# Performance work log

Measured on AMD Instinct MI355X. Metric: run time of the kernel, lower is better.

## Reference

```python
import jax, jax.numpy as jnp
import numpy as np

N_R = 256          # number of relations
N_HOP_MAX = 3      # max hops
N_E = 200_000      # number of entities
N_T = 1_000_000    # number of KB triples
B = 32             # batch size
D_Q = 768          # BERT question embedding dim
D_IN = D_Q + (N_HOP_MAX - 1) * N_R  # input width of dense_inf / dense_att


def setup_inputs() -> dict:
    key = jax.random.key(0)
    ks = jax.random.split(key, 7)
    x = (jax.random.uniform(ks[0], (B, N_E)) < 0.001).astype(jnp.float32)
    h_q = jax.random.normal(ks[1], (B, D_Q), jnp.float32)
    W_inf = jax.random.normal(ks[2], (N_R, D_IN), jnp.float32) * 0.02
    W_att = jax.random.normal(ks[3], (1, D_IN), jnp.float32) * 0.02
    subj_idx = jax.random.randint(ks[4], (N_T,), 0, N_E, jnp.int32)
    rel_idx = jax.random.randint(ks[5], (N_T,), 0, N_R, jnp.int32)
    obj_idx = jax.random.randint(ks[6], (N_T,), 0, N_E, jnp.int32)
    return {"x": x, "h_q": h_q, "W_inf": W_inf, "W_att": W_att,
            "subj_idx": subj_idx, "rel_idx": rel_idx, "obj_idx": obj_idx,
            "n_hop": N_HOP_MAX}


def _one_step(x, r, subj_idx, rel_idx, obj_idx):
    # Equivalent to ((x @ M_subj.T) * (r @ M_rel.T)) @ M_obj with 0/1
    # indicator matrices: gather - elementwise multiply - scatter-add.
    x_t = jnp.take(x, subj_idx, axis=1)   # (B, N_T)
    r_t = jnp.take(r, rel_idx, axis=1)    # (B, N_T)
    prod = x_t * r_t                       # (B, N_T)
    # scatter-add over triples into object entities: (N_T, B) -> (N_E, B)
    return jax.ops.segment_sum(prod.T, obj_idx, num_segments=x.shape[1]).T


def reference(x, h_q, W_inf, W_att, subj_idx, rel_idx, obj_idx, n_hop):
    rs, cs, xs = [], [], []
    for i in range(n_hop):
        if i:
            # most-recent relation first, then older ones (rs[::-1])
            concat = jnp.concatenate([h_q] + rs[::-1], axis=1)
        else:
            concat = h_q
        pad = jnp.zeros((h_q.shape[0], (N_HOP_MAX - 1 - i) * N_R), h_q.dtype)
        concat = jnp.concatenate([concat, pad], axis=1)  # (B, D_IN)
        r = concat @ W_inf.T   # (B, N_R)
        c = concat @ W_att.T   # (B, 1)
        x = _one_step(x, r, subj_idx, rel_idx, obj_idx)  # (B, N_E)
        rs.append(r)
        cs.append(c)
        xs.append(x)
    a = jax.nn.softmax(jnp.concatenate(cs, axis=1), axis=-1)  # (B, n_hop)
    y = jnp.einsum('bh,bhe->be', a, jnp.stack(xs, axis=1))     # (B, N_E)
    return y
```

## Files before the change

kernel.cpp:

```cpp
#include <hip/hip_runtime.h>

#define N_R   256
#define N_E   200000
#define N_T   1000000
#define D_Q   768
#define D_IN  1280

template <bool BN>
__device__ __forceinline__ void hop_quad(
        const float* __restrict__ xIn, const unsigned* __restrict__ maskIn,
        const float* __restrict__ rT,
        const int4* __restrict__ subj4, const int4* __restrict__ rel4,
        const int4* __restrict__ obj4,
        float* __restrict__ xOut, unsigned* __restrict__ maskOut,
        int gb, int t) {
    int tid = gb * 256 + t;
    if (tid >= N_T / 4) return;
    int4 s4 = subj4[tid];
    unsigned m0 = maskIn[s4.x], m1 = maskIn[s4.y];
    unsigned m2 = maskIn[s4.z], m3 = maskIn[s4.w];
    if (!(m0 | m1 | m2 | m3)) return;
    int4 r4 = rel4[tid];
    int4 o4 = obj4[tid];
    int      ss[4] = {s4.x, s4.y, s4.z, s4.w};
    unsigned mk[4] = {m0, m1, m2, m3};
    int      rr[4] = {r4.x, r4.y, r4.z, r4.w};
    int      oo[4] = {o4.x, o4.y, o4.z, o4.w};
#pragma unroll
    for (int k = 0; k < 4; ++k) {
        unsigned mm = mk[k];
        if (!mm) continue;
        int s = ss[k], o = oo[k];
        const float* rrow = rT + rr[k] * 32;
        while (mm) {
            int bb = __ffs(mm) - 1;
            mm &= mm - 1;
            float v = BN ? xIn[(size_t)bb * N_E + s] : xIn[(size_t)s * 32 + bb];
            unsafeAtomicAdd(&xOut[(size_t)o * 32 + bb], v * rrow[bb]);
        }
        atomicOr(&maskOut[o], mk[k]);
    }
}

__global__ void kA(const float* __restrict__ x, const float* __restrict__ h_q,
                   const float* __restrict__ W_inf,
                   unsigned* __restrict__ mask0, unsigned* __restrict__ mask1,
                   unsigned* __restrict__ mask2,
                   float4* __restrict__ outv, float* __restrict__ rT0) {
    __shared__ float hs[32 * 257];
    __shared__ float red[256];
    int t = threadIdx.x;
    if (blockIdx.x < 782) {
        int tid = blockIdx.x * 256 + t;
        float4 z = {0.f, 0.f, 0.f, 0.f};
        for (int i = tid; i < 1600000; i += 782 * 256) outv[i] = z;
        if (tid < N_E) {
            unsigned m = 0;
#pragma unroll 8
            for (int b = 0; b < 32; ++b)
                m |= (x[(size_t)b * N_E + tid] != 0.f ? 1u : 0u) << b;
            mask0[tid] = m;
            mask1[tid] = 0u;
            mask2[tid] = 0u;
        }
    } else {
        int rel = blockIdx.x - 782;
        int b = t & 31, kp = t >> 5;
        float acc = 0.f;
        for (int c = 0; c < 3; ++c) {
            __syncthreads();
#pragma unroll
            for (int i = 0; i < 32; ++i)
                hs[i * 257 + t] = h_q[i * D_Q + c * 256 + t];
            __syncthreads();
            const float* w = &W_inf[rel * D_IN + c * 256 + kp * 32];
#pragma unroll
            for (int i = 0; i < 32; ++i)
                acc += w[i] * hs[b * 257 + kp * 32 + i];
        }
        red[t] = acc;
        __syncthreads();
        if (t < 32) {
            float s = 0.f;
            for (int q = 0; q < 8; ++q) s += red[q * 32 + t];
            rT0[rel * 32 + t] = s;
        }
    }
}

__global__ void kB(const float* __restrict__ W_inf, const float* __restrict__ rT0,
                   float* __restrict__ rT1,
                   const float* __restrict__ x, const unsigned* __restrict__ mask0,
                   const int4* __restrict__ subj4, const int4* __restrict__ rel4,
                   const int4* __restrict__ obj4,
                   float* __restrict__ bufA, unsigned* __restrict__ mask1) {
    __shared__ float red[256];
    int t = threadIdx.x;
    if (blockIdx.x < 256) {
        int relb = blockIdx.x;
        int b = t & 31, jp = t >> 5;
        const float* w2 = &W_inf[relb * D_IN + D_Q];
        float acc = 0.f;
#pragma unroll 8
        for (int jj = 0; jj < 32; ++jj) {
            int j = jp * 32 + jj;
            acc += w2[j] * rT0[j * 32 + b];
        }
        red[t] = acc;
        __syncthreads();
        if (t < 32) {
            float s = rT0[relb * 32 + t];
            for (int q = 0; q < 8; ++q) s += red[q * 32 + t];
            rT1[relb * 32 + t] = s;
        }
    } else {
        hop_quad<true>(x, mask0, rT0, subj4, rel4, obj4, bufA, mask1,
                       blockIdx.x - 256, t);
    }
}

__global__ void kC(const float* __restrict__ W_inf, const float* __restrict__ W_att,
                   const float* __restrict__ h_q,
                   const float* __restrict__ rT0, const float* __restrict__ rT1,
                   float* __restrict__ rT2, float* __restrict__ a_w,
                   const float* __restrict__ bufA, const unsigned* __restrict__ mask1,
                   const int4* __restrict__ subj4, const int4* __restrict__ rel4,
                   const int4* __restrict__ obj4,
                   float* __restrict__ bufB, unsigned* __restrict__ mask2,
                   float* __restrict__ out) {
    __shared__ float red[256];
    __shared__ float p0[256], p1[256], p2[256], p3[256];
    int t = threadIdx.x;
    if (blockIdx.x < 256) {
        int relb = blockIdx.x;
        int b = t & 31, jp = t >> 5;
        const float* w2 = &W_inf[relb * D_IN + D_Q];
        const float* w3 = w2 + N_R;
        float acc = 0.f;
#pragma unroll 8
        for (int jj = 0; jj < 32; ++jj) {
            int j = jp * 32 + jj;
            acc += w2[j] * rT1[j * 32 + b] + w3[j] * rT0[j * 32 + b];
        }
        red[t] = acc;
        __syncthreads();
        if (t < 32) {
            float s = rT0[relb * 32 + t];
            for (int q = 0; q < 8; ++q) s += red[q * 32 + t];
            rT2[relb * 32 + t] = s;
        }
    } else if (blockIdx.x == 256) {
        int b = t & 31, p = t >> 5;
        float c0 = 0.f;
        for (int k = p * 96; k < p * 96 + 96; ++k) c0 += W_att[k] * h_q[b * D_Q + k];
        float s1 = 0.f, s2 = 0.f, s3 = 0.f;
        for (int j = p * 32; j < p * 32 + 32; ++j) {
            float w2 = W_att[D_Q + j], w3 = W_att[D_Q + N_R + j];
            float r0v = rT0[j * 32 + b], r1v = rT1[j * 32 + b];
            s1 += w2 * r0v; s2 += w2 * r1v; s3 += w3 * r0v;
        }
        p0[t] = c0; p1[t] = s1; p2[t] = s2; p3[t] = s3;
        __syncthreads();
        if (t < 32) {
            float C0 = 0.f, S1 = 0.f, S2 = 0.f, S3 = 0.f;
            for (int q = 0; q < 8; ++q) {
                C0 += p0[q * 32 + t]; S1 += p1[q * 32 + t];
                S2 += p2[q * 32 + t]; S3 += p3[q * 32 + t];
            }
            float c1 = C0 + S1, c2 = C0 + S2 + S3;
            float m  = fmaxf(C0, fmaxf(c1, c2));
            float e0 = __expf(C0 - m), e1 = __expf(c1 - m), e2 = __expf(c2 - m);
            float inv = 1.f / (e0 + e1 + e2);
            a_w[t] = e0 * inv; a_w[32 + t] = e1 * inv; a_w[64 + t] = e2 * inv;
        }
    } else if (blockIdx.x < 1234) {
        hop_quad<false>(bufA, mask1, rT1, subj4, rel4, obj4, bufB, mask2,
                        blockIdx.x - 257, t);
    } else {
        __shared__ float a0l[32];
        if (t < 32) {
            int b = t;
            float c0 = 0.f;
            for (int k = 0; k < D_Q; ++k) c0 += W_att[k] * h_q[b * D_Q + k];
            float s1 = 0.f, s2 = 0.f, s3 = 0.f;
            for (int j = 0; j < N_R; ++j) {
                float w2 = W_att[D_Q + j], w3 = W_att[D_Q + N_R + j];
                float r0v = rT0[j * 32 + b], r1v = rT1[j * 32 + b];
                s1 += w2 * r0v; s2 += w2 * r1v; s3 += w3 * r0v;
            }
            float C0 = c0, c1 = C0 + s1, c2 = C0 + s2 + s3;
            float m  = fmaxf(C0, fmaxf(c1, c2));
            float e0 = __expf(C0 - m), e1 = __expf(c1 - m), e2 = __expf(c2 - m);
            a0l[t] = e0 / (e0 + e1 + e2);
        }
        __syncthreads();
        int e = (blockIdx.x - 1234) * 256 + t;
        if (e >= N_E) return;
        unsigned m1v = mask1[e];
        if (!m1v) return;
        const float* r1 = bufA + (size_t)e * 32;
        while (m1v) {
            int bb = __ffs(m1v) - 1;
            m1v &= m1v - 1;
            unsafeAtomicAdd(&out[(size_t)bb * N_E + e], a0l[bb] * r1[bb]);
        }
    }
}

__global__ void kDE(const float* __restrict__ bufB,
                    const unsigned* __restrict__ mask2,
                    const float* __restrict__ rT2, const float* __restrict__ a_w,
                    const int2* __restrict__ subj2, const int2* __restrict__ rel2,
                    const int2* __restrict__ obj2, float* __restrict__ out) {
    __shared__ float a1s[32], a2s[32];
    int t = threadIdx.x;
    if (t < 32) { a1s[t] = a_w[32 + t]; a2s[t] = a_w[64 + t]; }
    __syncthreads();
    if (blockIdx.x < 1954) {
        int tid = blockIdx.x * 256 + t;
        if (tid >= N_T / 2) return;
        int2 s2 = subj2[tid];
        unsigned m0 = mask2[s2.x], m1 = mask2[s2.y];
        if (!(m0 | m1)) return;
        int2 r2 = rel2[tid];
        int2 o2 = obj2[tid];
        int      ss[2] = {s2.x, s2.y};
        unsigned mk[2] = {m0, m1};
        int      rr[2] = {r2.x, r2.y};
        int      oo[2] = {o2.x, o2.y};
#pragma unroll
        for (int k = 0; k < 2; ++k) {
            unsigned mm = mk[k];
            if (!mm) continue;
            const float* rrow = rT2 + rr[k] * 32;
            const float* xrow = bufB + (size_t)ss[k] * 32;
            int o = oo[k];
            while (mm) {
                int bb = __ffs(mm) - 1;
                mm &= mm - 1;
                unsafeAtomicAdd(&out[(size_t)bb * N_E + o],
                                a2s[bb] * xrow[bb] * rrow[bb]);
            }
        }
    } else {
        int e = (blockIdx.x - 1954) * 256 + t;
        if (e >= N_E) return;
        unsigned m2v = mask2[e];
        if (!m2v) return;
        const float* r2 = bufB + (size_t)e * 32;
        while (m2v) {
            int bb = __ffs(m2v) - 1;
            m2v &= m2v - 1;
            unsafeAtomicAdd(&out[(size_t)bb * N_E + e], a1s[bb] * r2[bb]);
        }
    }
}

extern "C" void kernel_launch(void* const* d_in, const int* in_sizes, int n_in,
                              void* d_out, int out_size, void* d_ws, size_t ws_size,
                              hipStream_t stream) {
    const float* x     = (const float*)d_in[0];
    const float* h_q   = (const float*)d_in[1];
    const float* W_inf = (const float*)d_in[2];
    const float* W_att = (const float*)d_in[3];
    const int*   subj  = (const int*)d_in[4];
    const int*   rel   = (const int*)d_in[5];
    const int*   obj   = (const int*)d_in[6];
    float* out = (float*)d_out;

    const size_t NEB = (size_t)N_E * 32;
    float*    bufA  = (float*)d_ws;
    float*    bufB  = bufA + NEB;
    float*    rT0   = bufB + NEB;
    float*    rT1   = rT0 + N_R * 32;
    float*    rT2   = rT1 + N_R * 32;
    float*    a_w   = rT2 + N_R * 32;
    unsigned* mask0 = (unsigned*)(a_w + 96);
    unsigned* mask1 = mask0 + N_E;
    unsigned* mask2 = mask1 + N_E;

    kA<<<782 + 256, 256, 0, stream>>>(x, h_q, W_inf, mask0, mask1, mask2,
                                      (float4*)out, rT0);
    kB<<<256 + 977, 256, 0, stream>>>(W_inf, rT0, rT1, x, mask0,
                                      (const int4*)subj, (const int4*)rel,
                                      (const int4*)obj, bufA, mask1);
    kC<<<257 + 977 + 782, 256, 0, stream>>>(W_inf, W_att, h_q, rT0, rT1, rT2,
                                            a_w, bufA, mask1, (const int4*)subj,
                                            (const int4*)rel, (const int4*)obj,
                                            bufB, mask2, out);
    kDE<<<1954 + 782, 256, 0, stream>>>(bufB, mask2, rT2, a_w,
                                        (const int2*)subj, (const int2*)rel,
                                        (const int2*)obj, out);
}
```

Measured before the change: 203.3 us.

## Precompute attention projection of W_inf to compute softmax weights one stage earlier

```diff
diff --git a/kernel.cpp b/kernel.cpp
--- a/kernel.cpp
+++ b/kernel.cpp
@@ -43,10 +43,11 @@
 }
 
 __global__ void kA(const float* __restrict__ x, const float* __restrict__ h_q,
-                   const float* __restrict__ W_inf,
+                   const float* __restrict__ W_inf, const float* __restrict__ W_att,
                    unsigned* __restrict__ mask0, unsigned* __restrict__ mask1,
                    unsigned* __restrict__ mask2,
-                   float4* __restrict__ outv, float* __restrict__ rT0) {
+                   float4* __restrict__ outv, float* __restrict__ rT0,
+                   float* __restrict__ u) {
     __shared__ float hs[32 * 257];
     __shared__ float red[256];
     int t = threadIdx.x;
@@ -63,7 +64,7 @@
             mask1[tid] = 0u;
             mask2[tid] = 0u;
         }
-    } else {
+    } else if (blockIdx.x < 1038) {
         int rel = blockIdx.x - 782;
         int b = t & 31, kp = t >> 5;
         float acc = 0.f;
@@ -85,16 +86,24 @@
             for (int q = 0; q < 8; ++q) s += red[q * 32 + t];
             rT0[rel * 32 + t] = s;
         }
-    }
-}
-
-__global__ void kB(const float* __restrict__ W_inf, const float* __restrict__ rT0,
-                   float* __restrict__ rT1,
+    } else {
+        float acc = 0.f;
+        for (int rel = 0; rel < N_R; ++rel)
+            acc += W_att[D_Q + rel] * W_inf[(size_t)rel * D_IN + D_Q + t];
+        u[t] = acc;
+    }
+}
+
+__global__ void kB(const float* __restrict__ W_inf, const float* __restrict__ W_att,
+                   const float* __restrict__ h_q, const float* __restrict__ u,
+                   const float* __restrict__ rT0, float* __restrict__ rT1,
+                   float* __restrict__ a_w,
                    const float* __restrict__ x, const unsigned* __restrict__ mask0,
                    const int4* __restrict__ subj4, const int4* __restrict__ rel4,
                    const int4* __restrict__ obj4,
                    float* __restrict__ bufA, unsigned* __restrict__ mask1) {
     __shared__ float red[256];
+    __shared__ float p0[256], p1[256], p2[256], p3[256];
     int t = threadIdx.x;
     if (blockIdx.x < 256) {
         int relb = blockIdx.x;
@@ -113,23 +122,47 @@
             for (int q = 0; q < 8; ++q) s += red[q * 32 + t];
             rT1[relb * 32 + t] = s;
         }
+    } else if (blockIdx.x == 256) {
+        int b = t & 31, p = t >> 5;
+        float c0 = 0.f;
+        for (int k = p * 96; k < p * 96 + 96; ++k) c0 += W_att[k] * h_q[b * D_Q + k];
+        float s1 = 0.f, su = 0.f, s3 = 0.f;
+        for (int j = p * 32; j < p * 32 + 32; ++j) {
+            float w2 = W_att[D_Q + j], w3 = W_att[D_Q + N_R + j];
+            float r0v = rT0[j * 32 + b];
+            s1 += w2 * r0v; su += u[j] * r0v; s3 += w3 * r0v;
+        }
+        p0[t] = c0; p1[t] = s1; p2[t] = su; p3[t] = s3;
+        __syncthreads();
+        if (t < 32) {
+            float C0 = 0.f, S1 = 0.f, SU = 0.f, S3 = 0.f;
+            for (int q = 0; q < 8; ++q) {
+                C0 += p0[q * 32 + t]; S1 += p1[q * 32 + t];
+                SU += p2[q * 32 + t]; S3 += p3[q * 32 + t];
+            }
+            float c1 = C0 + S1;
+            float c2 = C0 + S1 + SU + S3;
+            float m  = fmaxf(C0, fmaxf(c1, c2));
+            float e0 = __expf(C0 - m), e1 = __expf(c1 - m), e2 = __expf(c2 - m);
+            float inv = 1.f / (e0 + e1 + e2);
+            a_w[t] = e0 * inv; a_w[32 + t] = e1 * inv; a_w[64 + t] = e2 * inv;
+        }
     } else {
         hop_quad<true>(x, mask0, rT0, subj4, rel4, obj4, bufA, mask1,
-                       blockIdx.x - 256, t);
-    }
-}
-
-__global__ void kC(const float* __restrict__ W_inf, const float* __restrict__ W_att,
-                   const float* __restrict__ h_q,
+                       blockIdx.x - 257, t);
+    }
+}
+
+__global__ void kC(const float* __restrict__ W_inf,
                    const float* __restrict__ rT0, const float* __restrict__ rT1,
-                   float* __restrict__ rT2, float* __restrict__ a_w,
+                   float* __restrict__ rT2, const float* __restrict__ a_w,
                    const float* __restrict__ bufA, const unsigned* __restrict__ mask1,
                    const int4* __restrict__ subj4, const int4* __restrict__ rel4,
                    const int4* __restrict__ obj4,
                    float* __restrict__ bufB, unsigned* __restrict__ mask2,
                    float* __restrict__ out) {
     __shared__ float red[256];
-    __shared__ float p0[256], p1[256], p2[256], p3[256];
+    __shared__ float a0s[32];
     int t = threadIdx.x;
     if (blockIdx.x < 256) {
         int relb = blockIdx.x;
@@ -149,52 +182,13 @@
             for (int q = 0; q < 8; ++q) s += red[q * 32 + t];
             rT2[relb * 32 + t] = s;
         }
-    } else if (blockIdx.x == 256) {
-        int b = t & 31, p = t >> 5;
-        float c0 = 0.f;
-        for (int k = p * 96; k < p * 96 + 96; ++k) c0 += W_att[k] * h_q[b * D_Q + k];
-        float s1 = 0.f, s2 = 0.f, s3 = 0.f;
-        for (int j = p * 32; j < p * 32 + 32; ++j) {
-            float w2 = W_att[D_Q + j], w3 = W_att[D_Q + N_R + j];
-            float r0v = rT0[j * 32 + b], r1v = rT1[j * 32 + b];
-            s1 += w2 * r0v; s2 += w2 * r1v; s3 += w3 * r0v;
-        }
-        p0[t] = c0; p1[t] = s1; p2[t] = s2; p3[t] = s3;
-        __syncthreads();
-        if (t < 32) {
-            float C0 = 0.f, S1 = 0.f, S2 = 0.f, S3 = 0.f;
-            for (int q = 0; q < 8; ++q) {
-                C0 += p0[q * 32 + t]; S1 += p1[q * 32 + t];
-                S2 += p2[q * 32 + t]; S3 += p3[q * 32 + t];
-            }
-            float c1 = C0 + S1, c2 = C0 + S2 + S3;
-            float m  = fmaxf(C0, fmaxf(c1, c2));
-            float e0 = __expf(C0 - m), e1 = __expf(c1 - m), e2 = __expf(c2 - m);
-            float inv = 1.f / (e0 + e1 + e2);
-            a_w[t] = e0 * inv; a_w[32 + t] = e1 * inv; a_w[64 + t] = e2 * inv;
-        }
-    } else if (blockIdx.x < 1234) {
+    } else if (blockIdx.x < 1233) {
         hop_quad<false>(bufA, mask1, rT1, subj4, rel4, obj4, bufB, mask2,
-                        blockIdx.x - 257, t);
-    } else {
-        __shared__ float a0l[32];
-        if (t < 32) {
-            int b = t;
-            float c0 = 0.f;
-            for (int k = 0; k < D_Q; ++k) c0 += W_att[k] * h_q[b * D_Q + k];
-            float s1 = 0.f, s2 = 0.f, s3 = 0.f;
-            for (int j = 0; j < N_R; ++j) {
-                float w2 = W_att[D_Q + j], w3 = W_att[D_Q + N_R + j];
-                float r0v = rT0[j * 32 + b], r1v = rT1[j * 32 + b];
-                s1 += w2 * r0v; s2 += w2 * r1v; s3 += w3 * r0v;
-            }
-            float C0 = c0, c1 = C0 + s1, c2 = C0 + s2 + s3;
-            float m  = fmaxf(C0, fmaxf(c1, c2));
-            float e0 = __expf(C0 - m), e1 = __expf(c1 - m), e2 = __expf(c2 - m);
-            a0l[t] = e0 / (e0 + e1 + e2);
-        }
-        __syncthreads();
-        int e = (blockIdx.x - 1234) * 256 + t;
+                        blockIdx.x - 256, t);
+    } else {
+        if (t < 32) a0s[t] = a_w[t];
+        __syncthreads();
+        int e = (blockIdx.x - 1233) * 256 + t;
         if (e >= N_E) return;
         unsigned m1v = mask1[e];
         if (!m1v) return;
@@ -202,7 +196,7 @@
         while (m1v) {
             int bb = __ffs(m1v) - 1;
             m1v &= m1v - 1;
-            unsafeAtomicAdd(&out[(size_t)bb * N_E + e], a0l[bb] * r1[bb]);
+            unsafeAtomicAdd(&out[(size_t)bb * N_E + e], a0s[bb] * r1[bb]);
         }
     }
 }
@@ -275,17 +269,20 @@
     float*    rT1   = rT0 + N_R * 32;
     float*    rT2   = rT1 + N_R * 32;
     float*    a_w   = rT2 + N_R * 32;
-    unsigned* mask0 = (unsigned*)(a_w + 96);
+    float*    u     = a_w + 96;
+    unsigned* mask0 = (unsigned*)(u + 256);
     unsigned* mask1 = mask0 + N_E;
     unsigned* mask2 = mask1 + N_E;
 
-    kA<<<782 + 256, 256, 0, stream>>>(x, h_q, W_inf, mask0, mask1, mask2,
-                                      (float4*)out, rT0);
-    kB<<<256 + 977, 256, 0, stream>>>(W_inf, rT0, rT1, x, mask0,
-                                      (const int4*)subj, (const int4*)rel,
-                                      (const int4*)obj, bufA, mask1);
-    kC<<<257 + 977 + 782, 256, 0, stream>>>(W_inf, W_att, h_q, rT0, rT1, rT2,
-                                            a_w, bufA, mask1, (const int4*)subj,
+    kA<<<782 + 256 + 1, 256, 0, stream>>>(x, h_q, W_inf, W_att,
+                                          mask0, mask1, mask2,
+                                          (float4*)out, rT0, u);
+    kB<<<257 + 977, 256, 0, stream>>>(W_inf, W_att, h_q, u, rT0, rT1, a_w,
+                                      x, mask0, (const int4*)subj,
+                                      (const int4*)rel, (const int4*)obj,
+                                      bufA, mask1);
+    kC<<<256 + 977 + 782, 256, 0, stream>>>(W_inf, rT0, rT1, rT2, a_w,
+                                            bufA, mask1, (const int4*)subj,
                                             (const int4*)rel, (const int4*)obj,
                                             bufB, mask2, out);
     kDE<<<1954 + 782, 256, 0, stream>>>(bufB, mask2, rT2, a_w,
```

Measured after the change: 201.3 us. Within noise of the previous version (-1.0%).
